# Kernel optimization log

Hardware: AMD Instinct MI355X
Metric: run time of the kernel (lower is better)

## Reference

```python
import jax, jax.numpy as jnp
import numpy as np

D_MODEL = 1024
N_HEADS = 16
HEAD_DIM = D_MODEL // N_HEADS


def setup_inputs() -> dict:
    key = jax.random.key(0)
    ks = jax.random.split(key, 5)
    B, T = 4, 2048
    s_in = 1.0 / np.sqrt(D_MODEL)
    x = jax.random.normal(ks[0], (B, T, D_MODEL), dtype=jnp.float32)
    w_qkv = jax.random.normal(ks[1], (D_MODEL, 3 * D_MODEL), dtype=jnp.float32) * s_in
    b_qkv = jnp.zeros((3 * D_MODEL,), dtype=jnp.float32)
    w_proj = jax.random.normal(ks[2], (D_MODEL, D_MODEL), dtype=jnp.float32) * s_in
    b_proj = jnp.zeros((D_MODEL,), dtype=jnp.float32)
    return {"x": x, "w_qkv": w_qkv, "b_qkv": b_qkv, "w_proj": w_proj, "b_proj": b_proj}


def reference(x, w_qkv, b_qkv, w_proj, b_proj):
    B, T, D = x.shape
    H, Hd = N_HEADS, HEAD_DIM
    qkv = x @ w_qkv + b_qkv                       # [B,T,3D]
    qkv = qkv.reshape(B, T, 3, H, Hd)
    q = jnp.transpose(qkv[:, :, 0], (0, 2, 1, 3))  # [B,H,T,Hd]
    k = jnp.transpose(qkv[:, :, 1], (0, 2, 1, 3))
    v = jnp.transpose(qkv[:, :, 2], (0, 2, 1, 3))
    scale = 1.0 / np.sqrt(Hd).astype(np.float32)
    attn = jnp.einsum('bhqd,bhkd->bhqk', q, k) * scale  # [B,H,T,T]
    causal = jnp.tril(jnp.ones((T, T), dtype=bool))
    attn = jnp.where(causal[None, None], attn, -jnp.inf)
    attn = jax.nn.softmax(attn, axis=-1)
    out = jnp.einsum('bhqk,bhkd->bhqd', attn, v)  # [B,H,T,Hd]
    out = jnp.transpose(out, (0, 2, 1, 3)).reshape(B, T, D)
    return out @ w_proj + b_proj
```

## Files before the change

### kernel.cpp

```cpp
#include <hip/hip_runtime.h>
#include <math.h>
#include <stdint.h>

typedef unsigned short u16;
typedef __bf16 bf16x8 __attribute__((ext_vector_type(8)));
typedef float  f32x4  __attribute__((ext_vector_type(4)));

#define AS1 __attribute__((address_space(1)))
#define AS3 __attribute__((address_space(3)))

__device__ __forceinline__ void gld_lds16(const void* g, void* l) {
    __builtin_amdgcn_global_load_lds((AS1 const uint32_t*)g, (AS3 uint32_t*)l, 16, 0, 0);
}

__device__ __forceinline__ u16 f2bf(float f) {
    unsigned u = __float_as_uint(f);
    unsigned r = u + 0x7fffu + ((u >> 16) & 1u);
    return (u16)(r >> 16);
}

namespace {
constexpr int Tc  = 2048;
constexpr int Hc  = 16;
constexpr size_t QE = 8388608;
}

__global__ __launch_bounds__(256) void cvt_bf16(const float* __restrict__ in,
                                                u16* __restrict__ out, int n8) {
    int i = blockIdx.x * 256 + threadIdx.x;
    if (i >= n8) return;
    const float4* p = (const float4*)in + (size_t)i * 2;
    float4 a = p[0], b = p[1];
    union { u16 u[8]; uint4 v; } r;
    r.u[0] = f2bf(a.x); r.u[1] = f2bf(a.y); r.u[2] = f2bf(a.z); r.u[3] = f2bf(a.w);
    r.u[4] = f2bf(b.x); r.u[5] = f2bf(b.y); r.u[6] = f2bf(b.z); r.u[7] = f2bf(b.w);
    ((uint4*)out)[i] = r.v;
}

__global__ __launch_bounds__(256) void cvtT(const float* __restrict__ in,
                                            u16* __restrict__ out, int K, int N) {
    __shared__ u16 t[64][72];
    const int n0 = blockIdx.x * 64, k0 = blockIdx.y * 64;
    const int tid = threadIdx.x;
    const int r = tid >> 2, c0 = (tid & 3) << 4;
    const float* src = in + (size_t)(k0 + r) * N + n0 + c0;
#pragma unroll
    for (int j = 0; j < 16; j += 4) {
        float4 f = *(const float4*)(src + j);
        t[r][c0 + j + 0] = f2bf(f.x);
        t[r][c0 + j + 1] = f2bf(f.y);
        t[r][c0 + j + 2] = f2bf(f.z);
        t[r][c0 + j + 3] = f2bf(f.w);
    }
    __syncthreads();
    u16* dst = out + (size_t)(n0 + r) * K + k0 + c0;
    union { u16 u[8]; uint4 v; } o1, o2;
#pragma unroll
    for (int j = 0; j < 8; ++j) o1.u[j] = t[c0 + j][r];
#pragma unroll
    for (int j = 0; j < 8; ++j) o2.u[j] = t[c0 + 8 + j][r];
    *(uint4*)dst = o1.v;
    *(uint4*)(dst + 8) = o2.v;
}

__global__ __launch_bounds__(256) void qkv_gemm_bf16(
    const u16* __restrict__ xb, const u16* __restrict__ wT,
    const float* __restrict__ bias,
    u16* __restrict__ qo, u16* __restrict__ ko, u16* __restrict__ vt)
{
    __shared__ u16 At[2][4096];
    __shared__ u16 Bt[2][4096];

    const int tid  = threadIdx.x;
    const int lane = tid & 63;
    const int wv   = tid >> 6;
    const int wr   = wv >> 1;
    const int wc   = wv & 1;
    const int m0   = blockIdx.x * 128;
    const int n0   = blockIdx.y * 128;

    const int p1 = wv * 128 + lane, p2 = p1 + 64;
    const int r1 = p1 >> 2, c1 = (p1 & 3) ^ ((r1 >> 1) & 3);
    const int r2 = p2 >> 2, c2 = (p2 & 3) ^ ((r2 >> 1) & 3);

    const u16* ga1 = xb + (size_t)(m0 + r1) * 1024 + c1 * 8;
    const u16* ga2 = xb + (size_t)(m0 + r2) * 1024 + c2 * 8;
    const u16* gb1 = wT + (size_t)(n0 + r1) * 1024 + c1 * 8;
    const u16* gb2 = wT + (size_t)(n0 + r2) * 1024 + c2 * 8;

    f32x4 acc[4][4] = {};

#define STAGE_G(buf, k0)                                   \
    do {                                                   \
        gld_lds16(ga1 + (k0), &At[buf][wv * 1024]);        \
        gld_lds16(ga2 + (k0), &At[buf][wv * 1024 + 512]);  \
        gld_lds16(gb1 + (k0), &Bt[buf][wv * 1024]);        \
        gld_lds16(gb2 + (k0), &Bt[buf][wv * 1024 + 512]);  \
    } while (0)

    STAGE_G(0, 0);
    asm volatile("s_waitcnt vmcnt(0)" ::: "memory");
    __syncthreads();

    int cur = 0;
    for (int t = 0; t < 32; ++t) {
        if (t < 31) STAGE_G(cur ^ 1, (t + 1) * 32);
        bf16x8 af[4], bfr[4];
#pragma unroll
        for (int i = 0; i < 4; ++i) {
            int row = wr * 64 + i * 16 + (lane & 15);
            int c   = (lane >> 4) ^ ((row >> 1) & 3);
            af[i] = *(const bf16x8*)&At[cur][row * 32 + c * 8];
            int rowb = wc * 64 + i * 16 + (lane & 15);
            int cb   = (lane >> 4) ^ ((rowb >> 1) & 3);
            bfr[i] = *(const bf16x8*)&Bt[cur][rowb * 32 + cb * 8];
        }
#pragma unroll
        for (int i = 0; i < 4; ++i)
#pragma unroll
            for (int j = 0; j < 4; ++j)
                acc[i][j] = __builtin_amdgcn_mfma_f32_16x16x32_bf16(
                    af[i], bfr[j], acc[i][j], 0, 0, 0);
        asm volatile("s_waitcnt vmcnt(0)" ::: "memory");
        __syncthreads();
        cur ^= 1;
    }
#undef STAGE_G

    const int nq = n0 + wc * 64;
    const int which = nq >> 10;
    const int h  = (nq & 1023) >> 6;
    const int rr = (lane >> 4) * 4;
    const int cl = lane & 15;

    if (which < 2) {
        u16* dst = which ? ko : qo;
#pragma unroll
        for (int i = 0; i < 4; ++i)
#pragma unroll
            for (int j = 0; j < 4; ++j) {
                int d = j * 16 + cl;
                float bv = bias[nq + d];
#pragma unroll
                for (int r = 0; r < 4; ++r) {
                    int m = m0 + wr * 64 + i * 16 + rr + r;
                    int b = m >> 11, tt = m & 2047;
                    dst[(((size_t)(b * Hc + h)) * Tc + tt) * 64 + d] =
                        f2bf(acc[i][j][r] + bv);
                }
            }
    } else {
#pragma unroll
        for (int i = 0; i < 4; ++i) {
            int m = m0 + wr * 64 + i * 16 + rr;
            int b = m >> 11, tt = m & 2047;
#pragma unroll
            for (int j = 0; j < 4; ++j) {
                int d = j * 16 + cl;
                float bv = bias[nq + d];
                union { u16 u[4]; uint2 v2; } pk;
#pragma unroll
                for (int r = 0; r < 4; ++r) pk.u[r] = f2bf(acc[i][j][r] + bv);
                *(uint2*)&vt[((size_t)(b * Hc + h) * 64 + d) * Tc + tt] = pk.v2;
            }
        }
    }
}

__global__ __launch_bounds__(256, 3) void flash_mfma(
    const u16* __restrict__ qg, const u16* __restrict__ kg,
    const u16* __restrict__ vtg, u16* __restrict__ og)
{
    __shared__ u16 Ks[2][4096];
    __shared__ u16 Vs[2][4096];
    __shared__ u16 Ps[8192];

    const int tid  = threadIdx.x;
    const int lane = tid & 63;
    const int wv   = tid >> 6;
    const int qb   = 15 - (int)(blockIdx.x >> 6);
    const int bh   = blockIdx.x & 63;

    const int p1 = wv * 128 + lane, p2 = p1 + 64;
    const int r1 = p1 >> 3, c1 = (p1 & 7) ^ (r1 & 7);
    const int r2 = p2 >> 3, c2 = (p2 & 7) ^ (r2 & 7);

    const size_t tb = (size_t)bh * Tc;
    const u16* kb1 = kg + (tb + r1) * 64 + c1 * 8;
    const u16* kb2 = kg + (tb + r2) * 64 + c2 * 8;
    const u16* vb1 = vtg + ((size_t)bh * 64 + r1) * Tc + c1 * 8;
    const u16* vb2 = vtg + ((size_t)bh * 64 + r2) * Tc + c2 * 8;

    bf16x8 qr[2][2];
    {
        const u16* qbase = qg + (tb + (size_t)qb * 128 + wv * 32) * 64;
#pragma unroll
        for (int ar = 0; ar < 2; ++ar)
#pragma unroll
            for (int ks = 0; ks < 2; ++ks) {
                union { bf16x8 v; u16 u[8]; uint4 q; } t;
                t.q = *(const uint4*)(qbase + (ar * 16 + (lane & 15)) * 64 +
                                      ks * 32 + (lane >> 4) * 8);
#pragma unroll
                for (int j = 0; j < 8; ++j) {
                    float f = __uint_as_float((unsigned)t.u[j] << 16) * 0.125f;
                    t.u[j] = f2bf(f);
                }
                qr[ar][ks] = t.v;
            }
    }

    gld_lds16(kb1, &Ks[0][wv * 1024]);
    gld_lds16(kb2, &Ks[0][wv * 1024 + 512]);
    gld_lds16(vb1, &Vs[0][wv * 1024]);
    gld_lds16(vb2, &Vs[0][wv * 1024 + 512]);
    asm volatile("s_waitcnt vmcnt(0)" ::: "memory");
    __syncthreads();

    f32x4 accO[2][4] = {};
    float mi[2][4], li[2][4];
#pragma unroll
    for (int a = 0; a < 2; ++a)
#pragma unroll
        for (int r = 0; r < 4; ++r) { mi[a][r] = -INFINITY; li[a][r] = 0.f; }

    const int nt = 2 * qb + 2;
    int cur = 0;

    for (int kt = 0; kt < nt; ++kt) {
        if (kt + 1 < nt) {
            int nx = kt + 1;
            gld_lds16(kb1 + (size_t)nx * 4096, &Ks[cur ^ 1][wv * 1024]);
            gld_lds16(kb2 + (size_t)nx * 4096, &Ks[cur ^ 1][wv * 1024 + 512]);
            gld_lds16(vb1 + nx * 64, &Vs[cur ^ 1][wv * 1024]);
            gld_lds16(vb2 + nx * 64, &Vs[cur ^ 1][wv * 1024 + 512]);
        }

        const bool skip = (kt == 2 * qb + 1) && (wv < 2);
        if (!skip) {
            f32x4 s4[2][4] = {};
            __builtin_amdgcn_s_setprio(1);
#pragma unroll
            for (int ks = 0; ks < 2; ++ks) {
                bf16x8 bk[4];
#pragma unroll
                for (int nf = 0; nf < 4; ++nf) {
                    int brow = nf * 16 + (lane & 15);
                    int bc   = (ks * 4 + (lane >> 4)) ^ (brow & 7);
                    bk[nf] = *(const bf16x8*)&Ks[cur][brow * 64 + bc * 8];
                }
#pragma unroll
                for (int ar = 0; ar < 2; ++ar)
#pragma unroll
                    for (int nf = 0; nf < 4; ++nf)
                        s4[ar][nf] = __builtin_amdgcn_mfma_f32_16x16x32_bf16(
                            qr[ar][ks], bk[nf], s4[ar][nf], 0, 0, 0);
            }
            __builtin_amdgcn_s_setprio(0);

            if (kt >= 2 * qb) {
#pragma unroll
                for (int ar = 0; ar < 2; ++ar)
#pragma unroll
                    for (int nf = 0; nf < 4; ++nf)
#pragma unroll
                        for (int r = 0; r < 4; ++r) {
                            int key  = kt * 64 + nf * 16 + (lane & 15);
                            int qrow = qb * 128 + wv * 32 + ar * 16 +
                                       (lane >> 4) * 4 + r;
                            if (key > qrow) s4[ar][nf][r] = -INFINITY;
                        }
            }

#pragma unroll
            for (int ar = 0; ar < 2; ++ar)
#pragma unroll
                for (int r = 0; r < 4; ++r) {
                    float v0 = s4[ar][0][r], v1 = s4[ar][1][r];
                    float v2 = s4[ar][2][r], v3 = s4[ar][3][r];
                    float rm = fmaxf(fmaxf(v0, v1), fmaxf(v2, v3));
#pragma unroll
                    for (int off = 8; off; off >>= 1)
                        rm = fmaxf(rm, __shfl_xor(rm, off, 16));
                    float mnew = fmaxf(mi[ar][r], rm);
                    float sc = __expf(mi[ar][r] - mnew);
                    float pv0 = __expf(v0 - mnew), pv1 = __expf(v1 - mnew);
                    float pv2 = __expf(v2 - mnew), pv3 = __expf(v3 - mnew);
                    float rs = pv0 + pv1 + pv2 + pv3;
#pragma unroll
                    for (int off = 8; off; off >>= 1)
                        rs += __shfl_xor(rs, off, 16);
                    li[ar][r] = li[ar][r] * sc + rs;
                    mi[ar][r] = mnew;
#pragma unroll
                    for (int df = 0; df < 4; ++df) accO[ar][df][r] *= sc;

                    int lrow = ar * 16 + (lane >> 4) * 4 + r;
                    int rb   = wv * 2048 + lrow * 64;
                    int k0c  = lane & 15;
                    Ps[rb + (((0 * 16 + k0c) >> 3) ^ (lrow & 7)) * 8 + (k0c & 7)] = f2bf(pv0);
                    Ps[rb + (((1 * 16 + k0c) >> 3) ^ (lrow & 7)) * 8 + (k0c & 7)] = f2bf(pv1);
                    Ps[rb + (((2 * 16 + k0c) >> 3) ^ (lrow & 7)) * 8 + (k0c & 7)] = f2bf(pv2);
                    Ps[rb + (((3 * 16 + k0c) >> 3) ^ (lrow & 7)) * 8 + (k0c & 7)] = f2bf(pv3);
                }

            __builtin_amdgcn_s_setprio(1);
#pragma unroll
            for (int ks = 0; ks < 2; ++ks) {
                bf16x8 ap[2];
#pragma unroll
                for (int ar = 0; ar < 2; ++ar) {
                    int arow = ar * 16 + (lane & 15);
                    int ac   = (ks * 4 + (lane >> 4)) ^ (arow & 7);
                    ap[ar] = *(const bf16x8*)&Ps[wv * 2048 + arow * 64 + ac * 8];
                }
#pragma unroll
                for (int df = 0; df < 4; ++df) {
                    int brow = df * 16 + (lane & 15);
                    int bc   = (ks * 4 + (lane >> 4)) ^ (brow & 7);
                    bf16x8 bv = *(const bf16x8*)&Vs[cur][brow * 64 + bc * 8];
#pragma unroll
                    for (int ar = 0; ar < 2; ++ar)
                        accO[ar][df] = __builtin_amdgcn_mfma_f32_16x16x32_bf16(
                            ap[ar], bv, accO[ar][df], 0, 0, 0);
                }
            }
            __builtin_amdgcn_s_setprio(0);
        }

        asm volatile("s_waitcnt vmcnt(0)" ::: "memory");
        __syncthreads();
        cur ^= 1;
    }

#pragma unroll
    for (int ar = 0; ar < 2; ++ar)
#pragma unroll
        for (int r = 0; r < 4; ++r) {
            float inv = 1.0f / li[ar][r];
            int t = qb * 128 + wv * 32 + ar * 16 + (lane >> 4) * 4 + r;
#pragma unroll
            for (int df = 0; df < 4; ++df) {
                int d = df * 16 + (lane & 15);
                og[(tb + t) * 64 + d] = f2bf(accO[ar][df][r] * inv);
            }
        }
}

__global__ __launch_bounds__(256) void proj_gemm_bf16(
    const u16* __restrict__ ob, const u16* __restrict__ wT,
    const float* __restrict__ bias, float* __restrict__ out)
{
    __shared__ u16 At[2][4096];
    __shared__ u16 Bt[2][4096];

    const int tid  = threadIdx.x;
    const int lane = tid & 63;
    const int wv   = tid >> 6;
    const int wr   = wv >> 1;
    const int wc   = wv & 1;
    const int m0   = blockIdx.x * 128;
    const int n0   = blockIdx.y * 128;

    const int p1 = wv * 128 + lane, p2 = p1 + 64;
    const int r1 = p1 >> 2, c1 = (p1 & 3) ^ ((r1 >> 1) & 3);
    const int r2 = p2 >> 2, c2 = (p2 & 3) ^ ((r2 >> 1) & 3);

    const int m1 = m0 + r1, m2 = m0 + r2;
    const size_t ab1 = ((size_t)(m1 >> 11) * Hc) * Tc + (m1 & 2047);
    const size_t ab2 = ((size_t)(m2 >> 11) * Hc) * Tc + (m2 & 2047);
    const u16* gb1 = wT + (size_t)(n0 + r1) * 1024 + c1 * 8;
    const u16* gb2 = wT + (size_t)(n0 + r2) * 1024 + c2 * 8;

    f32x4 acc[4][4] = {};

#define STAGE_P(buf, k0)                                                          \
    do {                                                                          \
        int kk1 = (k0) + c1 * 8, kk2 = (k0) + c2 * 8;                             \
        gld_lds16(ob + (ab1 + (size_t)(kk1 >> 6) * Tc) * 64 + (kk1 & 63),         \
                  &At[buf][wv * 1024]);                                           \
        gld_lds16(ob + (ab2 + (size_t)(kk2 >> 6) * Tc) * 64 + (kk2 & 63),         \
                  &At[buf][wv * 1024 + 512]);                                     \
        gld_lds16(gb1 + (k0), &Bt[buf][wv * 1024]);                               \
        gld_lds16(gb2 + (k0), &Bt[buf][wv * 1024 + 512]);                         \
    } while (0)

    STAGE_P(0, 0);
    asm volatile("s_waitcnt vmcnt(0)" ::: "memory");
    __syncthreads();

    int cur = 0;
    for (int t = 0; t < 32; ++t) {
        if (t < 31) STAGE_P(cur ^ 1, (t + 1) * 32);
        bf16x8 af[4], bfr[4];
#pragma unroll
        for (int i = 0; i < 4; ++i) {
            int row = wr * 64 + i * 16 + (lane & 15);
            int c   = (lane >> 4) ^ ((row >> 1) & 3);
            af[i] = *(const bf16x8*)&At[cur][row * 32 + c * 8];
            int rowb = wc * 64 + i * 16 + (lane & 15);
            int cb   = (lane >> 4) ^ ((rowb >> 1) & 3);
            bfr[i] = *(const bf16x8*)&Bt[cur][rowb * 32 + cb * 8];
        }
#pragma unroll
        for (int i = 0; i < 4; ++i)
#pragma unroll
            for (int j = 0; j < 4; ++j)
                acc[i][j] = __builtin_amdgcn_mfma_f32_16x16x32_bf16(
                    af[i], bfr[j], acc[i][j], 0, 0, 0);
        asm volatile("s_waitcnt vmcnt(0)" ::: "memory");
        __syncthreads();
        cur ^= 1;
    }
#undef STAGE_P

    const int rr = (lane >> 4) * 4;
    const int cl = lane & 15;
#pragma unroll
    for (int i = 0; i < 4; ++i)
#pragma unroll
        for (int j = 0; j < 4; ++j) {
            int n = n0 + wc * 64 + j * 16 + cl;
            float bv = bias[n];
#pragma unroll
            for (int r = 0; r < 4; ++r) {
                int m = m0 + wr * 64 + i * 16 + rr + r;
                out[(size_t)m * 1024 + n] = acc[i][j][r] + bv;
            }
        }
}

extern "C" void kernel_launch(void* const* d_in, const int* in_sizes, int n_in,
                              void* d_out, int out_size, void* d_ws, size_t ws_size,
                              hipStream_t stream) {
    const float* x      = (const float*)d_in[0];
    const float* w_qkv  = (const float*)d_in[1];
    const float* b_qkv  = (const float*)d_in[2];
    const float* w_proj = (const float*)d_in[3];
    const float* b_proj = (const float*)d_in[4];
    float* out = (float*)d_out;

    u16* xb     = (u16*)d_ws;
    u16* wqkvT  = xb + QE;
    u16* wprojT = wqkvT + 3145728;
    u16* qb16   = wprojT + 1048576;
    u16* kb16   = qb16 + QE;
    u16* vtb    = kb16 + QE;
    u16* ob16   = vtb + QE;

    cvt_bf16<<<4096, 256, 0, stream>>>(x, xb, 1048576);
    cvtT<<<dim3(48, 16), 256, 0, stream>>>(w_qkv, wqkvT, 1024, 3072);
    cvtT<<<dim3(16, 16), 256, 0, stream>>>(w_proj, wprojT, 1024, 1024);
    qkv_gemm_bf16<<<dim3(64, 24), 256, 0, stream>>>(xb, wqkvT, b_qkv, qb16, kb16, vtb);
    flash_mfma<<<1024, 256, 0, stream>>>(qb16, kb16, vtb, ob16);
    proj_gemm_bf16<<<dim3(64, 8), 256, 0, stream>>>(ob16, wprojT, b_proj, out);
}
```

Before: 322.4 us.

## Triple-buffer GEMM loads with one barrier per step; defer softmax row-sum reduction

Both the QKV and projection GEMMs move from double to triple LDS buffering. Two K-slices stay in flight, the wait is partial (vmcnt(4)) and each iteration needs only one barrier instead of a full drain. In the attention kernel, the per-iteration shuffle reduction of the softmax row sum is removed. Each lane keeps a partial sum, and the sums are reduced once before normalization. This costs more LDS per block (48KB) in exchange for more load/compute overlap and less shuffle work in the inner loop.

```diff
diff --git a/kernel.cpp b/kernel.cpp
--- a/kernel.cpp
+++ b/kernel.cpp
@@ -68,8 +68,8 @@
     const float* __restrict__ bias,
     u16* __restrict__ qo, u16* __restrict__ ko, u16* __restrict__ vt)
 {
-    __shared__ u16 At[2][4096];
-    __shared__ u16 Bt[2][4096];
+    __shared__ u16 At[3][4096];
+    __shared__ u16 Bt[3][4096];
 
     const int tid  = threadIdx.x;
     const int lane = tid & 63;
@@ -98,22 +98,16 @@
         gld_lds16(gb2 + (k0), &Bt[buf][wv * 1024 + 512]);  \
     } while (0)
 
-    STAGE_G(0, 0);
-    asm volatile("s_waitcnt vmcnt(0)" ::: "memory");
-    __syncthreads();
-
-    int cur = 0;
-    for (int t = 0; t < 32; ++t) {
-        if (t < 31) STAGE_G(cur ^ 1, (t + 1) * 32);
+    auto COMPUTE = [&](int bsel) {
         bf16x8 af[4], bfr[4];
 #pragma unroll
         for (int i = 0; i < 4; ++i) {
             int row = wr * 64 + i * 16 + (lane & 15);
             int c   = (lane >> 4) ^ ((row >> 1) & 3);
-            af[i] = *(const bf16x8*)&At[cur][row * 32 + c * 8];
+            af[i] = *(const bf16x8*)&At[bsel][row * 32 + c * 8];
             int rowb = wc * 64 + i * 16 + (lane & 15);
             int cb   = (lane >> 4) ^ ((rowb >> 1) & 3);
-            bfr[i] = *(const bf16x8*)&Bt[cur][rowb * 32 + cb * 8];
+            bfr[i] = *(const bf16x8*)&Bt[bsel][rowb * 32 + cb * 8];
         }
 #pragma unroll
         for (int i = 0; i < 4; ++i)
@@ -121,10 +115,23 @@
             for (int j = 0; j < 4; ++j)
                 acc[i][j] = __builtin_amdgcn_mfma_f32_16x16x32_bf16(
                     af[i], bfr[j], acc[i][j], 0, 0, 0);
-        asm volatile("s_waitcnt vmcnt(0)" ::: "memory");
-        __syncthreads();
-        cur ^= 1;
-    }
+    };
+
+    STAGE_G(0, 0);
+    STAGE_G(1, 32);
+    int b0 = 0, b1 = 1, b2 = 2;
+    for (int t = 0; t < 31; ++t) {
+        asm volatile("s_waitcnt vmcnt(4)" ::: "memory");
+        __builtin_amdgcn_s_barrier();
+        asm volatile("" ::: "memory");
+        if (t < 30) STAGE_G(b2, (t + 2) * 32);
+        COMPUTE(b0);
+        int tmp = b0; b0 = b1; b1 = b2; b2 = tmp;
+    }
+    asm volatile("s_waitcnt vmcnt(0)" ::: "memory");
+    __builtin_amdgcn_s_barrier();
+    asm volatile("" ::: "memory");
+    COMPUTE(b0);
 #undef STAGE_G
 
     const int nq = n0 + wc * 64;
@@ -286,11 +293,7 @@
                     float sc = __expf(mi[ar][r] - mnew);
                     float pv0 = __expf(v0 - mnew), pv1 = __expf(v1 - mnew);
                     float pv2 = __expf(v2 - mnew), pv3 = __expf(v3 - mnew);
-                    float rs = pv0 + pv1 + pv2 + pv3;
-#pragma unroll
-                    for (int off = 8; off; off >>= 1)
-                        rs += __shfl_xor(rs, off, 16);
-                    li[ar][r] = li[ar][r] * sc + rs;
+                    li[ar][r] = li[ar][r] * sc + (pv0 + pv1 + pv2 + pv3);
                     mi[ar][r] = mnew;
 #pragma unroll
                     for (int df = 0; df < 4; ++df) accO[ar][df][r] *= sc;
@@ -337,7 +340,11 @@
     for (int ar = 0; ar < 2; ++ar)
 #pragma unroll
         for (int r = 0; r < 4; ++r) {
-            float inv = 1.0f / li[ar][r];
+            float lsum = li[ar][r];
+#pragma unroll
+            for (int off = 8; off; off >>= 1)
+                lsum += __shfl_xor(lsum, off, 16);
+            float inv = 1.0f / lsum;
             int t = qb * 128 + wv * 32 + ar * 16 + (lane >> 4) * 4 + r;
 #pragma unroll
             for (int df = 0; df < 4; ++df) {
@@ -351,8 +358,8 @@
     const u16* __restrict__ ob, const u16* __restrict__ wT,
     const float* __restrict__ bias, float* __restrict__ out)
 {
-    __shared__ u16 At[2][4096];
-    __shared__ u16 Bt[2][4096];
+    __shared__ u16 At[3][4096];
+    __shared__ u16 Bt[3][4096];
 
     const int tid  = threadIdx.x;
     const int lane = tid & 63;
@@ -385,22 +392,16 @@
         gld_lds16(gb2 + (k0), &Bt[buf][wv * 1024 + 512]);                         \
     } while (0)
 
-    STAGE_P(0, 0);
-    asm volatile("s_waitcnt vmcnt(0)" ::: "memory");
-    __syncthreads();
-
-    int cur = 0;
-    for (int t = 0; t < 32; ++t) {
-        if (t < 31) STAGE_P(cur ^ 1, (t + 1) * 32);
+    auto COMPUTE = [&](int bsel) {
         bf16x8 af[4], bfr[4];
 #pragma unroll
         for (int i = 0; i < 4; ++i) {
             int row = wr * 64 + i * 16 + (lane & 15);
             int c   = (lane >> 4) ^ ((row >> 1) & 3);
-            af[i] = *(const bf16x8*)&At[cur][row * 32 + c * 8];
+            af[i] = *(const bf16x8*)&At[bsel][row * 32 + c * 8];
             int rowb = wc * 64 + i * 16 + (lane & 15);
             int cb   = (lane >> 4) ^ ((rowb >> 1) & 3);
-            bfr[i] = *(const bf16x8*)&Bt[cur][rowb * 32 + cb * 8];
+            bfr[i] = *(const bf16x8*)&Bt[bsel][rowb * 32 + cb * 8];
         }
 #pragma unroll
         for (int i = 0; i < 4; ++i)
@@ -408,10 +409,23 @@
             for (int j = 0; j < 4; ++j)
                 acc[i][j] = __builtin_amdgcn_mfma_f32_16x16x32_bf16(
                     af[i], bfr[j], acc[i][j], 0, 0, 0);
-        asm volatile("s_waitcnt vmcnt(0)" ::: "memory");
-        __syncthreads();
-        cur ^= 1;
-    }
+    };
+
+    STAGE_P(0, 0);
+    STAGE_P(1, 32);
+    int b0 = 0, b1 = 1, b2 = 2;
+    for (int t = 0; t < 31; ++t) {
+        asm volatile("s_waitcnt vmcnt(4)" ::: "memory");
+        __builtin_amdgcn_s_barrier();
+        asm volatile("" ::: "memory");
+        if (t < 30) STAGE_P(b2, (t + 2) * 32);
+        COMPUTE(b0);
+        int tmp = b0; b0 = b1; b1 = b2; b2 = tmp;
+    }
+    asm volatile("s_waitcnt vmcnt(0)" ::: "memory");
+    __builtin_amdgcn_s_barrier();
+    asm volatile("" ::: "memory");
+    COMPUTE(b0);
 #undef STAGE_P
 
     const int rr = (lane >> 4) * 4;
```

Result: faster. 297.9 us (-7.6%).
